# Kernel optimization log

Hardware: AMD Instinct MI355X
Metric: run time of the kernel (lower is better)

The kernel has to match this reference:

```python
import jax, jax.numpy as jnp
import numpy as np

T, B, D = 2048, 32, 1024
AH, H = 128, 8
N, N2 = D // H, AH // H


def setup_inputs() -> dict:
    key = jax.random.key(0)
    ks = jax.random.split(key, 7)
    s1 = 1.0 / np.sqrt(N)
    s2 = 1.0 / np.sqrt(N2)
    return {
        "hyp": jax.random.normal(ks[0], (T, B, D), dtype=jnp.float32),
        "W_w": jax.random.uniform(ks[1], (N2, N), jnp.float32, -s1, s1),
        "W_b": jax.random.uniform(ks[2], (N2,), jnp.float32, -s1, s1),
        "Wm_w": jax.random.uniform(ks[3], (N2, N), jnp.float32, -s1, s1),
        "Wm_b": jax.random.uniform(ks[4], (N2,), jnp.float32, -s1, s1),
        "Wh_w": jax.random.uniform(ks[5], (1, N2), jnp.float32, -s2, s2),
        "Wh_b": jax.random.uniform(ks[6], (1,), jnp.float32, -s2, s2),
        "dan_hidden_size": D,
        "attention_hidden_size": AH,
        "multihead_size": H,
    }


def reference(hyp, W_w, W_b, Wm_w, Wm_b, Wh_w, Wh_b,
              dan_hidden_size, attention_hidden_size, multihead_size):
    t, b, d = hyp.shape
    h_ = multihead_size
    n = d // h_
    # (T,B,D) -> (B,H,T,N); weights are shared across heads in the original loop
    x = jnp.transpose(hyp.reshape(t, b, h_, n), (1, 2, 0, 3))
    m = x.mean(axis=2, keepdims=True)                      # (B,H,1,N) mean over time
    gate_x = jnp.tanh(jnp.einsum('bhtn,kn->bhtk', x, W_w) + W_b)
    gate_m = jnp.tanh(jnp.einsum('bhtn,kn->bhtk', m, Wm_w) + Wm_b)
    hgate = gate_x * gate_m                                 # (B,H,T,N2)
    logits = jnp.einsum('bhtk,ok->bhto', hgate, Wh_w) + Wh_b  # (B,H,T,1)
    a = jax.nn.softmax(logits, axis=2)                      # softmax over time
    c = jnp.sum(a * x, axis=2)                              # (B,H,N)
    return c.reshape(b, h_ * n)
```

## Files before the change

kernel.cpp:

```cpp
#include <hip/hip_runtime.h>
#include <hip/hip_fp16.h>
#include <math.h>

#define T_   2048
#define B_   32
#define D_   1024
#define H_   8
#define N_   128
#define NK   16
#define TSPL 8
#define TBLK (T_/TSPL)
#define BD4  (B_*D_/4)
#define APS  132
#define LOG2E 1.4426950408889634f

typedef __attribute__((ext_vector_type(8))) _Float16 half8;
typedef __attribute__((ext_vector_type(4))) float f32x4;

__device__ __forceinline__ half8 to_half8(float4 a, float4 b) {
    half8 r;
    r[0] = (_Float16)a.x; r[1] = (_Float16)a.y;
    r[2] = (_Float16)a.z; r[3] = (_Float16)a.w;
    r[4] = (_Float16)b.x; r[5] = (_Float16)b.y;
    r[6] = (_Float16)b.z; r[7] = (_Float16)b.w;
    return r;
}

__device__ __forceinline__ float tanh_fast(float d) {
    return 1.f - 2.f * __frcp_rn(exp2f(d * (2.f * LOG2E)) + 1.f);
}

#define LOADX(dst, step_) { \
    const int trow_ = t0 + (step_) * 64 + w * 16 + kk; \
    const size_t rb_ = (size_t)trow_ * BD4 + base4; \
    (dst)[0] = hyp4[rb_ + g * 2];      (dst)[1] = hyp4[rb_ + g * 2 + 1]; \
    (dst)[2] = hyp4[rb_ + 8 + g * 2];  (dst)[3] = hyp4[rb_ + 8 + g * 2 + 1]; \
    (dst)[4] = hyp4[rb_ + 16 + g * 2]; (dst)[5] = hyp4[rb_ + 16 + g * 2 + 1]; \
    (dst)[6] = hyp4[rb_ + 24 + g * 2]; (dst)[7] = hyp4[rb_ + 24 + g * 2 + 1]; }

__global__ __launch_bounds__(256, 4) void k_p(const float* __restrict__ hyp,
                                              const float* __restrict__ Ww,
                                              const float* __restrict__ Wb,
                                              float* __restrict__ part,
                                              __half* __restrict__ Pbuf) {
    __shared__ float red[4 * N_];
    __shared__ __half Pl[TBLK * NK];
    const int tid  = threadIdx.x;
    const int lane = tid & 63;
    const int w    = tid >> 6;
    const int blk  = blockIdx.x;
    const int bh   = blk >> 3;
    const int spl  = blk & 7;
    const int b = bh >> 3, h = bh & 7;
    const int t0 = spl * TBLK;
    const float4* hyp4 = (const float4*)hyp;
    const float4* Ww4  = (const float4*)Ww;
    const int base4 = b * (D_ / 4) + h * (N_ / 4);
    const int kk = lane & 15;
    const int g  = lane >> 4;

    half8 wf[4];
#pragma unroll
    for (int ks = 0; ks < 4; ++ks) {
        float4 wa  = Ww4[kk * 32 + ks * 8 + g * 2];
        float4 wb4 = Ww4[kk * 32 + ks * 8 + g * 2 + 1];
        wf[ks] = to_half8(wa, wb4);
    }
    const float wbr = Wb[kk];

    float4 cs[8];
#pragma unroll
    for (int m = 0; m < 8; ++m) cs[m] = make_float4(0.f, 0.f, 0.f, 0.f);

#pragma unroll
    for (int step = 0; step < 4; ++step) {
        float4 xq[8];
        LOADX(xq, step);
#pragma unroll
        for (int m = 0; m < 8; ++m) {
            cs[m].x += xq[m].x; cs[m].y += xq[m].y;
            cs[m].z += xq[m].z; cs[m].w += xq[m].w;
        }
        f32x4 acc = {0.f, 0.f, 0.f, 0.f};
#pragma unroll
        for (int ks = 0; ks < 4; ++ks) {
            half8 xf = to_half8(xq[2*ks], xq[2*ks+1]);
            acc = __builtin_amdgcn_mfma_f32_16x16x32_f16(xf, wf[ks], acc, 0, 0, 0);
        }
        const int tl = step * 64 + w * 16 + g * 4;
#pragma unroll
        for (int i = 0; i < 4; ++i)
            Pl[(tl + i) * NK + kk] = __float2half(tanh_fast(acc[i] + wbr));
    }
    __syncthreads();
    {
        const uint4* src = (const uint4*)Pl;
        uint4* dst = (uint4*)(Pbuf + ((size_t)bh * T_ + t0) * NK);
        dst[tid]       = src[tid];
        dst[tid + 256] = src[tid + 256];
    }
#pragma unroll
    for (int m = 0; m < 8; ++m) {
#pragma unroll
        for (int mask = 1; mask <= 8; mask <<= 1) {
            cs[m].x += __shfl_xor(cs[m].x, mask, 64);
            cs[m].y += __shfl_xor(cs[m].y, mask, 64);
            cs[m].z += __shfl_xor(cs[m].z, mask, 64);
            cs[m].w += __shfl_xor(cs[m].w, mask, 64);
        }
    }
    if (kk == 0) {
#pragma unroll
        for (int m = 0; m < 8; ++m) {
            int nb = 32 * (m >> 1) + 8 * g + 4 * (m & 1);
            red[w * N_ + nb + 0] = cs[m].x;
            red[w * N_ + nb + 1] = cs[m].y;
            red[w * N_ + nb + 2] = cs[m].z;
            red[w * N_ + nb + 3] = cs[m].w;
        }
    }
    __syncthreads();
    if (tid < N_)
        part[blk * N_ + tid] = (red[tid] + red[N_ + tid])
                             + (red[2*N_ + tid] + red[3*N_ + tid]);
}

__global__ __launch_bounds__(256, 4) void k_att(const float* __restrict__ hyp,
                                                const float* __restrict__ part,
                                                const float* __restrict__ Wmw,
                                                const float* __restrict__ Wmb,
                                                const float* __restrict__ Whw,
                                                const __half* __restrict__ Pbuf,
                                                float* __restrict__ attp) {
    __shared__ float red[4 * N_];
    __shared__ float zred[4];
    __shared__ float m_l[N_];
    __shared__ float gw_l[NK];
    const int tid  = threadIdx.x;
    const int lane = tid & 63;
    const int w    = tid >> 6;
    const int j    = (int)blockIdx.x;
    const int blk  = (j & 7) + 8 * (255 - (j >> 3));
    const int bh   = blk >> 3;
    const int spl  = blk & 7;
    const int b = bh >> 3, h = bh & 7;
    const int t0 = spl * TBLK;
    const float4* hyp4 = (const float4*)hyp;
    const int base4 = b * (D_ / 4) + h * (N_ / 4);
    const int kk = lane & 15;
    const int g  = lane >> 4;

    if (tid < N_) {
        float s = 0.f;
#pragma unroll
        for (int s8 = 0; s8 < TSPL; ++s8) s += part[(bh * TSPL + s8) * N_ + tid];
        m_l[tid] = s * (1.f / (float)T_);
    }
    __syncthreads();
    if (tid < N_) {
        int k = tid >> 3, g3 = tid & 7;
        float dsum = 0.f;
#pragma unroll
        for (int i = 0; i < 16; ++i) {
            int n = g3 * 16 + i;
            dsum = fmaf(m_l[n], Wmw[k * N_ + n], dsum);
        }
        dsum += __shfl_xor(dsum, 1, 64);
        dsum += __shfl_xor(dsum, 2, 64);
        dsum += __shfl_xor(dsum, 4, 64);
        if (g3 == 0) gw_l[k] = tanhf(dsum + Wmb[k]) * Whw[k];
    }
    __syncthreads();
    float gmv[NK];
#pragma unroll
    for (int jq = 0; jq < NK; ++jq) gmv[jq] = gw_l[jq];

    float4 cacc[8];
#pragma unroll
    for (int m = 0; m < 8; ++m) cacc[m] = make_float4(0.f, 0.f, 0.f, 0.f);
    float zacc = 0.f;

#pragma unroll
    for (int step = 0; step < 4; ++step) {
        const int tr = t0 + step * 64 + w * 16 + kk;
        union { uint4 u; __half2 h[8]; } P0, P1;
        const uint4* pv = (const uint4*)(Pbuf + (size_t)(bh * T_ + tr) * NK);
        P0.u = pv[0]; P1.u = pv[1];
        float4 xq[8];
        LOADX(xq, step);
        float lg = 0.f;
#pragma unroll
        for (int q = 0; q < 4; ++q) {
            float2 f0 = __half22float2(P0.h[q]);
            float2 f1 = __half22float2(P1.h[q]);
            lg = fmaf(f0.x, gmv[2*q + 0], lg);
            lg = fmaf(f0.y, gmv[2*q + 1], lg);
            lg = fmaf(f1.x, gmv[8 + 2*q + 0], lg);
            lg = fmaf(f1.y, gmv[8 + 2*q + 1], lg);
        }
        float e = exp2f(lg * LOG2E);
        zacc += e;
#pragma unroll
        for (int m = 0; m < 8; ++m) {
            cacc[m].x = fmaf(e, xq[m].x, cacc[m].x);
            cacc[m].y = fmaf(e, xq[m].y, cacc[m].y);
            cacc[m].z = fmaf(e, xq[m].z, cacc[m].z);
            cacc[m].w = fmaf(e, xq[m].w, cacc[m].w);
        }
    }
#pragma unroll
    for (int m = 0; m < 8; ++m) {
#pragma unroll
        for (int mask = 1; mask <= 8; mask <<= 1) {
            cacc[m].x += __shfl_xor(cacc[m].x, mask, 64);
            cacc[m].y += __shfl_xor(cacc[m].y, mask, 64);
            cacc[m].z += __shfl_xor(cacc[m].z, mask, 64);
            cacc[m].w += __shfl_xor(cacc[m].w, mask, 64);
        }
    }
    float z = zacc;
    z += __shfl_xor(z, 1, 64);
    z += __shfl_xor(z, 2, 64);
    z += __shfl_xor(z, 4, 64);
    z += __shfl_xor(z, 8, 64);
    if (kk == 0) {
#pragma unroll
        for (int m = 0; m < 8; ++m) {
            int nb = 32 * (m >> 1) + 8 * g + 4 * (m & 1);
            red[w * N_ + nb + 0] = cacc[m].x;
            red[w * N_ + nb + 1] = cacc[m].y;
            red[w * N_ + nb + 2] = cacc[m].z;
            red[w * N_ + nb + 3] = cacc[m].w;
        }
    }
    if (lane == 0) zred[w] = z;
    __syncthreads();
    if (tid < N_) {
        attp[(size_t)blk * APS + tid] =
            (red[tid] + red[N_ + tid]) + (red[2*N_ + tid] + red[3*N_ + tid]);
    } else if (tid == N_) {
        attp[(size_t)blk * APS + N_] =
            (zred[0] + zred[1]) + (zred[2] + zred[3]);
    }
}

__global__ __launch_bounds__(128) void k_red(const float* __restrict__ attp,
                                             float* __restrict__ out) {
    int bh = blockIdx.x, tid = threadIdx.x;
    float Z = 0.f, c = 0.f;
#pragma unroll
    for (int s = 0; s < TSPL; ++s) {
        const float* pp = &attp[(size_t)(bh * TSPL + s) * APS];
        Z += pp[N_];
        c += pp[tid];
    }
    out[bh * N_ + tid] = c / Z;
}

extern "C" void kernel_launch(void* const* d_in, const int* in_sizes, int n_in,
                              void* d_out, int out_size, void* d_ws, size_t ws_size,
                              hipStream_t stream) {
    const float* hyp = (const float*)d_in[0];
    const float* Ww  = (const float*)d_in[1];
    const float* Wb  = (const float*)d_in[2];
    const float* Wmw = (const float*)d_in[3];
    const float* Wmb = (const float*)d_in[4];
    const float* Whw = (const float*)d_in[5];
    float* out  = (float*)d_out;
    float* part = (float*)d_ws;
    float* attp = part + 2048 * N_;
    __half* Pbuf = (__half*)((char*)d_ws + (4 << 20));

    k_p  <<<dim3(B_ * H_ * TSPL), 256, 0, stream>>>(hyp, Ww, Wb, part, Pbuf);
    k_att<<<dim3(B_ * H_ * TSPL), 256, 0, stream>>>(hyp, part, Wmw, Wmb, Whw,
                                                    Pbuf, attp);
    k_red<<<dim3(B_ * H_), 128, 0, stream>>>(attp, out);
}
```

Measured before the change: 108.0 us.

## Restructure attention kernel: compute weights into LDS, then column-parallel weighted sum

The attention kernel now computes one softmax weight per timestep per thread (256 rows per block), stores the weights in shared memory and reduces the block total with a full wave shuffle. The weighted sum is then computed with each thread owning one float4 column and a 32-row time group, so the heavy per-column shuffle reductions are replaced by a small shared-memory reduction across 8 groups. This removes many cross-lane shuffles and register pressure from the old layout, at the cost of an extra barrier and a different hyp access pattern in which each thread walks strided rows.

```diff
diff --git a/kernel.cpp b/kernel.cpp
--- a/kernel.cpp
+++ b/kernel.cpp
@@ -132,10 +132,11 @@
                                                 const float* __restrict__ Whw,
                                                 const __half* __restrict__ Pbuf,
                                                 float* __restrict__ attp) {
-    __shared__ float red[4 * N_];
-    __shared__ float zred[4];
     __shared__ float m_l[N_];
     __shared__ float gw_l[NK];
+    __shared__ float wexp_l[TBLK];
+    __shared__ float4 red4[8][32];
+    __shared__ float zred[4];
     const int tid  = threadIdx.x;
     const int lane = tid & 63;
     const int w    = tid >> 6;
@@ -147,8 +148,6 @@
     const int t0 = spl * TBLK;
     const float4* hyp4 = (const float4*)hyp;
     const int base4 = b * (D_ / 4) + h * (N_ / 4);
-    const int kk = lane & 15;
-    const int g  = lane >> 4;
 
     if (tid < N_) {
         float s = 0.f;
@@ -171,74 +170,58 @@
         if (g3 == 0) gw_l[k] = tanhf(dsum + Wmb[k]) * Whw[k];
     }
     __syncthreads();
-    float gmv[NK];
-#pragma unroll
-    for (int jq = 0; jq < NK; ++jq) gmv[jq] = gw_l[jq];
-
-    float4 cacc[8];
-#pragma unroll
-    for (int m = 0; m < 8; ++m) cacc[m] = make_float4(0.f, 0.f, 0.f, 0.f);
-    float zacc = 0.f;
-
-#pragma unroll
-    for (int step = 0; step < 4; ++step) {
-        const int tr = t0 + step * 64 + w * 16 + kk;
-        union { uint4 u; __half2 h[8]; } P0, P1;
-        const uint4* pv = (const uint4*)(Pbuf + (size_t)(bh * T_ + tr) * NK);
-        P0.u = pv[0]; P1.u = pv[1];
-        float4 xq[8];
-        LOADX(xq, step);
+
+    {
+        const uint4* pv = (const uint4*)(Pbuf + ((size_t)bh * T_ + t0) * NK);
+        union { uint4 u; __half2 hh[4]; } Pa, Pb;
+        Pa.u = pv[2 * tid];
+        Pb.u = pv[2 * tid + 1];
         float lg = 0.f;
 #pragma unroll
         for (int q = 0; q < 4; ++q) {
-            float2 f0 = __half22float2(P0.h[q]);
-            float2 f1 = __half22float2(P1.h[q]);
-            lg = fmaf(f0.x, gmv[2*q + 0], lg);
-            lg = fmaf(f0.y, gmv[2*q + 1], lg);
-            lg = fmaf(f1.x, gmv[8 + 2*q + 0], lg);
-            lg = fmaf(f1.y, gmv[8 + 2*q + 1], lg);
+            float2 f0 = __half22float2(Pa.hh[q]);
+            float2 f1 = __half22float2(Pb.hh[q]);
+            lg = fmaf(f0.x, gw_l[2*q + 0], lg);
+            lg = fmaf(f0.y, gw_l[2*q + 1], lg);
+            lg = fmaf(f1.x, gw_l[8 + 2*q + 0], lg);
+            lg = fmaf(f1.y, gw_l[8 + 2*q + 1], lg);
         }
         float e = exp2f(lg * LOG2E);
-        zacc += e;
-#pragma unroll
-        for (int m = 0; m < 8; ++m) {
-            cacc[m].x = fmaf(e, xq[m].x, cacc[m].x);
-            cacc[m].y = fmaf(e, xq[m].y, cacc[m].y);
-            cacc[m].z = fmaf(e, xq[m].z, cacc[m].z);
-            cacc[m].w = fmaf(e, xq[m].w, cacc[m].w);
-        }
-    }
-#pragma unroll
-    for (int m = 0; m < 8; ++m) {
-#pragma unroll
-        for (int mask = 1; mask <= 8; mask <<= 1) {
-            cacc[m].x += __shfl_xor(cacc[m].x, mask, 64);
-            cacc[m].y += __shfl_xor(cacc[m].y, mask, 64);
-            cacc[m].z += __shfl_xor(cacc[m].z, mask, 64);
-            cacc[m].w += __shfl_xor(cacc[m].w, mask, 64);
-        }
-    }
-    float z = zacc;
-    z += __shfl_xor(z, 1, 64);
-    z += __shfl_xor(z, 2, 64);
-    z += __shfl_xor(z, 4, 64);
-    z += __shfl_xor(z, 8, 64);
-    if (kk == 0) {
-#pragma unroll
-        for (int m = 0; m < 8; ++m) {
-            int nb = 32 * (m >> 1) + 8 * g + 4 * (m & 1);
-            red[w * N_ + nb + 0] = cacc[m].x;
-            red[w * N_ + nb + 1] = cacc[m].y;
-            red[w * N_ + nb + 2] = cacc[m].z;
-            red[w * N_ + nb + 3] = cacc[m].w;
-        }
-    }
-    if (lane == 0) zred[w] = z;
-    __syncthreads();
-    if (tid < N_) {
-        attp[(size_t)blk * APS + tid] =
-            (red[tid] + red[N_ + tid]) + (red[2*N_ + tid] + red[3*N_ + tid]);
-    } else if (tid == N_) {
+        wexp_l[tid] = e;
+        float z = e;
+        z += __shfl_xor(z, 1, 64);  z += __shfl_xor(z, 2, 64);
+        z += __shfl_xor(z, 4, 64);  z += __shfl_xor(z, 8, 64);
+        z += __shfl_xor(z, 16, 64); z += __shfl_xor(z, 32, 64);
+        if (lane == 0) zred[w] = z;
+    }
+    __syncthreads();
+
+    const int col4 = tid & 31, tg = tid >> 5;
+    float4 c0 = {0.f,0.f,0.f,0.f}, c1 = {0.f,0.f,0.f,0.f};
+    const float* we = &wexp_l[tg * 32];
+    const size_t rbase = (size_t)(t0 + tg * 32) * BD4 + base4 + col4;
+#pragma unroll
+    for (int i = 0; i < 32; i += 2) {
+        float w0 = we[i], w1 = we[i + 1];
+        float4 x0 = hyp4[rbase + (size_t)i * BD4];
+        float4 x1 = hyp4[rbase + (size_t)(i + 1) * BD4];
+        c0.x = fmaf(w0, x0.x, c0.x); c0.y = fmaf(w0, x0.y, c0.y);
+        c0.z = fmaf(w0, x0.z, c0.z); c0.w = fmaf(w0, x0.w, c0.w);
+        c1.x = fmaf(w1, x1.x, c1.x); c1.y = fmaf(w1, x1.y, c1.y);
+        c1.z = fmaf(w1, x1.z, c1.z); c1.w = fmaf(w1, x1.w, c1.w);
+    }
+    c0.x += c1.x; c0.y += c1.y; c0.z += c1.z; c0.w += c1.w;
+    red4[tg][col4] = c0;
+    __syncthreads();
+    if (tid < 32) {
+        float4 s = {0.f,0.f,0.f,0.f};
+#pragma unroll
+        for (int gg = 0; gg < 8; ++gg) {
+            float4 v = red4[gg][tid];
+            s.x += v.x; s.y += v.y; s.z += v.z; s.w += v.w;
+        }
+        *(float4*)&attp[(size_t)blk * APS + tid * 4] = s;
+    } else if (tid == 32) {
         attp[(size_t)blk * APS + N_] =
             (zred[0] + zred[1]) + (zred[2] + zred[3]);
     }
```

New measurement: 108.1 us. No clear change (+0.2%).
